# Optimization experiments

Hardware: AMD Instinct MI355X
Metric: run time of the kernel (lower is better)

Reference implementation:

```python
import jax, jax.numpy as jnp
import numpy as np

N_NODES = 50000
N_EDGES = 800000
D = 128
N_LAYERS = 4
NUM_GRAPHS = 128
BN_EPS = 1e-5


def setup_inputs() -> dict:
    key = jax.random.key(0)
    ks = jax.random.split(key, 10)
    x = jax.random.normal(ks[0], (N_NODES, D), dtype=jnp.float32)
    edge_index = jax.random.randint(ks[1], (2, N_EDGES), 0, N_NODES, dtype=jnp.int64)
    batch = jnp.sort(jax.random.randint(ks[2], (N_NODES,), 0, NUM_GRAPHS, dtype=jnp.int64))
    # GINConv MLP params: Linear(D->D), ReLU, Linear(D->D); stacked over layers.
    scale = 1.0 / np.sqrt(D)
    W1 = jax.random.normal(ks[3], (N_LAYERS, D, D), dtype=jnp.float32) * scale
    b1 = jnp.zeros((N_LAYERS, D), dtype=jnp.float32)
    W2 = jax.random.normal(ks[4], (N_LAYERS, D, D), dtype=jnp.float32) * scale
    b2 = jnp.zeros((N_LAYERS, D), dtype=jnp.float32)
    eps = jnp.zeros((N_LAYERS,), dtype=jnp.float32)  # train_eps=True, init 0
    bn_gamma = jnp.ones((N_LAYERS - 1, D), dtype=jnp.float32)
    bn_beta = jnp.zeros((N_LAYERS - 1, D), dtype=jnp.float32)
    return {"x": x, "edge_index": edge_index, "batch": batch,
            "W1": W1, "b1": b1, "W2": W2, "b2": b2, "eps": eps,
            "bn_gamma": bn_gamma, "bn_beta": bn_beta}


def reference(x, edge_index, batch, W1, b1, W2, b2, eps, bn_gamma, bn_beta):
    src, dst = edge_index[0], edge_index[1]
    h = x
    for i in range(N_LAYERS):
        # GINConv: MLP((1+eps)*x_i + sum_{j->i} x_j)
        agg = jax.ops.segment_sum(h[src], dst, num_segments=N_NODES)  # [N, D]
        z = (1.0 + eps[i]) * h + agg
        z = jnp.maximum(z @ W1[i] + b1[i], 0.0) @ W2[i] + b2[i]
        if i < N_LAYERS - 1:
            # BatchNorm1d (training-mode batch statistics) + ReLU
            mu = jnp.mean(z, axis=0)
            var = jnp.var(z, axis=0)
            z = (z - mu) * jax.lax.rsqrt(var + BN_EPS) * bn_gamma[i] + bn_beta[i]
            z = jnp.maximum(z, 0.0)
        h = z
    # global_add_pool
    return jax.ops.segment_sum(h, batch, num_segments=NUM_GRAPHS)  # [G, D]
```

## Files before the change

kernel.cpp:

```cpp
#include <hip/hip_runtime.h>

#define N_NODES 50000
#define N_EDGES 800000
#define D 128
#define NUM_GRAPHS 128

typedef __attribute__((ext_vector_type(8)))  short bfrag8;
typedef __attribute__((ext_vector_type(16))) float f32x16;

__device__ __forceinline__ float4 f4zero() { return make_float4(0.f, 0.f, 0.f, 0.f); }

__device__ __forceinline__ unsigned short f2bf(float f) {
    unsigned u = __float_as_uint(f);
    unsigned r = (u + 0x7fffu + ((u >> 16) & 1u)) >> 16;
    return (unsigned short)r;
}
__device__ __forceinline__ float bf2f(unsigned short b) {
    return __uint_as_float(((unsigned)b) << 16);
}
__device__ __forceinline__ void acc8(float* a, uint4 r) {
    a[0] += __uint_as_float(r.x << 16);
    a[1] += __uint_as_float(r.x & 0xffff0000u);
    a[2] += __uint_as_float(r.y << 16);
    a[3] += __uint_as_float(r.y & 0xffff0000u);
    a[4] += __uint_as_float(r.z << 16);
    a[5] += __uint_as_float(r.z & 0xffff0000u);
    a[6] += __uint_as_float(r.w << 16);
    a[7] += __uint_as_float(r.w & 0xffff0000u);
}

__global__ __launch_bounds__(256) void prep_kernel(
    const float* __restrict__ W1, const float* __restrict__ W2,
    const float* __restrict__ x, short* __restrict__ Wt,
    ushort4* __restrict__ Hb, unsigned* __restrict__ HcDummy,
    int* __restrict__ deg, float* __restrict__ stats,
    float* __restrict__ outZero)
{
    int b = blockIdx.x, t = threadIdx.x;
    if (b < 512) {
        int idx = b * 256 + t;
        int m = idx >> 14, rem = idx & 16383;
        int k = rem >> 7, n = rem & 127;
        const float* W = (m < 4) ? (W1 + (size_t)m * 16384)
                                 : (W2 + (size_t)(m - 4) * 16384);
        Wt[(size_t)m * 16384 + n * 128 + k] = (short)f2bf(W[k * 128 + n]);
    } else if (b < 6762) {
        int i = (b - 512) * 256 + t;
        float4 v = ((const float4*)x)[i];
        Hb[i] = make_ushort4(f2bf(v.x), f2bf(v.y), f2bf(v.z), f2bf(v.w));
    } else if (b < 6958) {
        int i = (b - 6762) * 256 + t;
        if (i < N_NODES) deg[i] = 0;
    } else if (b < 6982) {
        int i = (b - 6958) * 256 + t;
        stats[i] = 0.f;
    } else if (b < 7046) {
        int i = (b - 6982) * 256 + t;
        outZero[i] = 0.f;
    } else {
        if (t < 64)       ((unsigned*)Hb)[(size_t)N_NODES * 64 + t] = 0u;
        else if (t < 128) HcDummy[t - 64] = 0u;
    }
}

__global__ __launch_bounds__(256) void hist_kernel(
    const int* __restrict__ dst, int* __restrict__ deg,
    unsigned short* __restrict__ edge_pos)
{
    int e = blockIdx.x * 256 + threadIdx.x;
    if (e < N_EDGES) edge_pos[e] = (unsigned short)atomicAdd(&deg[dst[e]], 1);
}

__global__ __launch_bounds__(256) void scan_block_kernel(
    const int* __restrict__ deg, int* __restrict__ row_ptr,
    int* __restrict__ blockSum)
{
    __shared__ int wsum[4];
    int t = threadIdx.x, b = blockIdx.x;
    int i = b * 256 + t;
    int v = (i < N_NODES) ? ((deg[i] + 7) & ~7) : 0;
    int lane = t & 63, wid = t >> 6;
    #pragma unroll
    for (int off = 1; off < 64; off <<= 1) {
        int u = __shfl_up(v, off, 64);
        if (lane >= off) v += u;
    }
    if (lane == 63) wsum[wid] = v;
    __syncthreads();
    int add = 0;
    for (int w = 0; w < wid; ++w) add += wsum[w];
    v += add;
    if (i < N_NODES) row_ptr[i + 1] = v;
    if (t == 255) blockSum[b] = v;
}

__global__ __launch_bounds__(256) void scan_fixup_kernel(
    const int* __restrict__ blockSum, int* __restrict__ row_ptr, int nb)
{
    __shared__ int wsum[4];
    __shared__ int sbuf[256];
    int t = threadIdx.x, b = blockIdx.x;
    int v = (t < nb) ? blockSum[t] : 0;
    int lane = t & 63, wid = t >> 6;
    #pragma unroll
    for (int off = 1; off < 64; off <<= 1) {
        int u = __shfl_up(v, off, 64);
        if (lane >= off) v += u;
    }
    if (lane == 63) wsum[wid] = v;
    __syncthreads();
    int add = 0;
    for (int w = 0; w < wid; ++w) add += wsum[w];
    sbuf[t] = v + add;
    __syncthreads();
    if (b == 0 && t == 0) row_ptr[0] = 0;
    if (b > 0) {
        int off = sbuf[b - 1];
        int i = b * 256 + t;
        if (i < N_NODES) row_ptr[i + 1] += off;
    }
}

__global__ __launch_bounds__(256) void fill_kernel(
    const int* __restrict__ src, const int* __restrict__ dst,
    const int* __restrict__ row_ptr, const unsigned short* __restrict__ edge_pos,
    const int* __restrict__ deg, unsigned short* __restrict__ csr_src)
{
    int b = blockIdx.x, t = threadIdx.x;
    if (b < 3125) {
        int e = b * 256 + t;
        if (e < N_EDGES)
            csr_src[row_ptr[dst[e]] + (int)edge_pos[e]] = (unsigned short)src[e];
    } else {
        int n = (b - 3125) * 256 + t;
        if (n < N_NODES) {
            int e0 = row_ptr[n] + deg[n];
            int e1 = row_ptr[n + 1];
            for (int j = e0; j < e1; ++j)
                csr_src[j] = (unsigned short)N_NODES;
        }
    }
}

__global__ __launch_bounds__(256) void bnapply_kernel(
    uint4* __restrict__ H, const float* __restrict__ stats,
    const float* __restrict__ gamma, const float* __restrict__ beta)
{
    __shared__ float sa[128], sb[128];
    int tid = threadIdx.x;
    if (tid < 128) {
        float s = 0.f, q = 0.f;
        #pragma unroll
        for (int k = 0; k < 8; ++k) {
            s += stats[k * 256 + tid];
            q += stats[k * 256 + 128 + tid];
        }
        const float invN = 1.0f / (float)N_NODES;
        float m = s * invN;
        float a = gamma[tid] * rsqrtf(q * invN - m * m + 1e-5f);
        sa[tid] = a;
        sb[tid] = beta[tid] - m * a;
    }
    __syncthreads();
    int id = blockIdx.x * 256 + tid;
    int c0 = (id & 15) * 8;
    uint4 u = H[id];
    float lo, hi;
    lo = fmaxf(sa[c0 + 0] * __uint_as_float(u.x << 16)          + sb[c0 + 0], 0.f);
    hi = fmaxf(sa[c0 + 1] * __uint_as_float(u.x & 0xffff0000u) + sb[c0 + 1], 0.f);
    u.x = (unsigned)f2bf(lo) | ((unsigned)f2bf(hi) << 16);
    lo = fmaxf(sa[c0 + 2] * __uint_as_float(u.y << 16)          + sb[c0 + 2], 0.f);
    hi = fmaxf(sa[c0 + 3] * __uint_as_float(u.y & 0xffff0000u) + sb[c0 + 3], 0.f);
    u.y = (unsigned)f2bf(lo) | ((unsigned)f2bf(hi) << 16);
    lo = fmaxf(sa[c0 + 4] * __uint_as_float(u.z << 16)          + sb[c0 + 4], 0.f);
    hi = fmaxf(sa[c0 + 5] * __uint_as_float(u.z & 0xffff0000u) + sb[c0 + 5], 0.f);
    u.z = (unsigned)f2bf(lo) | ((unsigned)f2bf(hi) << 16);
    lo = fmaxf(sa[c0 + 6] * __uint_as_float(u.w << 16)          + sb[c0 + 6], 0.f);
    hi = fmaxf(sa[c0 + 7] * __uint_as_float(u.w & 0xffff0000u) + sb[c0 + 7], 0.f);
    u.w = (unsigned)f2bf(lo) | ((unsigned)f2bf(hi) << 16);
    H[id] = u;
}

__global__ __launch_bounds__(256, 3) void layer_kernel(
    const ushort* __restrict__ Hin,
    const int* __restrict__ row_ptr,
    const unsigned short* __restrict__ csr,
    const float* __restrict__ epsp,
    const short* __restrict__ Wt1,
    const short* __restrict__ Wt2,
    const float* __restrict__ bias1,
    const float* __restrict__ bias2,
    ushort* __restrict__ Hout,
    float* __restrict__ statsBase,
    const int* __restrict__ batch,
    float* __restrict__ poolOut,
    int M)
{
    __shared__ __align__(16) short Wlds[128 * 128];
    __shared__ __align__(16) short zlds[2][32 * 128];
    __shared__ float ssum[128];
    __shared__ float ssq[128];

    const int tid  = threadIdx.x;
    const int wv   = tid >> 6;
    const int lane = tid & 63;
    const int half = lane >> 5;
    const int ln   = lane & 31;
    const int rg   = wv & 1;
    const int ch   = wv >> 1;
    const int row0 = blockIdx.x * 64 + rg * 32;
    const bool doStats = (statsBase != nullptr);
    if (doStats && tid < 128) { ssum[tid] = 0.f; ssq[tid] = 0.f; }

    short* zw = &zlds[rg][0];

    {
        const uint4* H4 = (const uint4*)Hin;
        const float eps1 = 1.0f + *epsp;
        const int gl = tid & 15;
        #pragma unroll
        for (int it = 0; it < 4; ++it) {
            int r = it * 16 + (tid >> 4);
            int node = blockIdx.x * 64 + r;
            float acc[8] = {0.f, 0.f, 0.f, 0.f, 0.f, 0.f, 0.f, 0.f};
            if (node < M) {
                uint4 hv = H4[(size_t)node * 16 + gl];
                acc[0] = eps1 * __uint_as_float(hv.x << 16);
                acc[1] = eps1 * __uint_as_float(hv.x & 0xffff0000u);
                acc[2] = eps1 * __uint_as_float(hv.y << 16);
                acc[3] = eps1 * __uint_as_float(hv.y & 0xffff0000u);
                acc[4] = eps1 * __uint_as_float(hv.z << 16);
                acc[5] = eps1 * __uint_as_float(hv.z & 0xffff0000u);
                acc[6] = eps1 * __uint_as_float(hv.w << 16);
                acc[7] = eps1 * __uint_as_float(hv.w & 0xffff0000u);
                int beg = row_ptr[node], end = row_ptr[node + 1];
                int base = beg;
                int idx = (int)csr[base + gl];
                while (base < end) {
                    int nb = base + 16;
                    int nidx = 0;
                    if (nb < end) nidx = (int)csr[nb + gl];
                    int cnt = end - base;
                    int s0 = __shfl(idx, 0, 16), s1 = __shfl(idx, 1, 16);
                    int s2 = __shfl(idx, 2, 16), s3 = __shfl(idx, 3, 16);
                    int s4 = __shfl(idx, 4, 16), s5 = __shfl(idx, 5, 16);
                    int s6 = __shfl(idx, 6, 16), s7 = __shfl(idx, 7, 16);
                    uint4 u0 = H4[(size_t)s0 * 16 + gl];
                    uint4 u1 = H4[(size_t)s1 * 16 + gl];
                    uint4 u2 = H4[(size_t)s2 * 16 + gl];
                    uint4 u3 = H4[(size_t)s3 * 16 + gl];
                    uint4 u4 = H4[(size_t)s4 * 16 + gl];
                    uint4 u5 = H4[(size_t)s5 * 16 + gl];
                    uint4 u6 = H4[(size_t)s6 * 16 + gl];
                    uint4 u7 = H4[(size_t)s7 * 16 + gl];
                    if (cnt > 8) {
                        int t0 = __shfl(idx,  8, 16), t1 = __shfl(idx,  9, 16);
                        int t2 = __shfl(idx, 10, 16), t3 = __shfl(idx, 11, 16);
                        int t4 = __shfl(idx, 12, 16), t5 = __shfl(idx, 13, 16);
                        int t6 = __shfl(idx, 14, 16), t7 = __shfl(idx, 15, 16);
                        uint4 w0 = H4[(size_t)t0 * 16 + gl];
                        uint4 w1 = H4[(size_t)t1 * 16 + gl];
                        uint4 w2 = H4[(size_t)t2 * 16 + gl];
                        uint4 w3 = H4[(size_t)t3 * 16 + gl];
                        uint4 w4 = H4[(size_t)t4 * 16 + gl];
                        uint4 w5 = H4[(size_t)t5 * 16 + gl];
                        uint4 w6 = H4[(size_t)t6 * 16 + gl];
                        uint4 w7 = H4[(size_t)t7 * 16 + gl];
                        acc8(acc, u0); acc8(acc, u1); acc8(acc, u2); acc8(acc, u3);
                        acc8(acc, u4); acc8(acc, u5); acc8(acc, u6); acc8(acc, u7);
                        acc8(acc, w0); acc8(acc, w1); acc8(acc, w2); acc8(acc, w3);
                        acc8(acc, w4); acc8(acc, w5); acc8(acc, w6); acc8(acc, w7);
                    } else {
                        acc8(acc, u0); acc8(acc, u1); acc8(acc, u2); acc8(acc, u3);
                        acc8(acc, u4); acc8(acc, u5); acc8(acc, u6); acc8(acc, u7);
                    }
                    idx = nidx; base = nb;
                }
            }
            uint4 o;
            o.x = (unsigned)f2bf(acc[0]) | ((unsigned)f2bf(acc[1]) << 16);
            o.y = (unsigned)f2bf(acc[2]) | ((unsigned)f2bf(acc[3]) << 16);
            o.z = (unsigned)f2bf(acc[4]) | ((unsigned)f2bf(acc[5]) << 16);
            o.w = (unsigned)f2bf(acc[6]) | ((unsigned)f2bf(acc[7]) << 16);
            int rl = r & 31;
            ((uint4*)&zlds[r >> 5][0])[rl * 16 + (gl ^ (rl & 15))] = o;
        }
    }
    __syncthreads();

    bfrag8 af[8];
    #pragma unroll
    for (int kk = 0; kk < 8; ++kk) {
        int c = kk * 2 + half;
        af[kk] = *(const bfrag8*)(zw + ln * 128 + ((c ^ (ln & 15)) << 3));
    }
    {
        const int4* Wg = (const int4*)Wt1;
        int4* Wl = (int4*)Wlds;
        #pragma unroll
        for (int i = 0; i < 8; ++i) {
            int id = i * 256 + tid;
            int n = id >> 4, c = id & 15;
            Wl[n * 16 + (c ^ (n & 15))] = Wg[id];
        }
    }
    __syncthreads();

    {
        f32x16 acc[2];
        #pragma unroll
        for (int ci = 0; ci < 2; ++ci)
            #pragma unroll
            for (int r = 0; r < 16; ++r) acc[ci][r] = 0.f;

        #pragma unroll
        for (int kk = 0; kk < 8; ++kk) {
            #pragma unroll
            for (int ci = 0; ci < 2; ++ci) {
                int n = (ch * 2 + ci) * 32 + ln;
                int c = kk * 2 + half;
                bfrag8 bf = *(const bfrag8*)(Wlds + n * 128 + ((c ^ (n & 15)) << 3));
                acc[ci] = __builtin_amdgcn_mfma_f32_32x32x16_bf16(
                    af[kk], bf, acc[ci], 0, 0, 0);
            }
        }
        #pragma unroll
        for (int ci = 0; ci < 2; ++ci) {
            int col = (ch * 2 + ci) * 32 + ln;
            int cc = col >> 3, co = col & 7;
            float bv = bias1[col];
            #pragma unroll
            for (int r = 0; r < 16; ++r) {
                int rloc = (r & 3) + 8 * (r >> 2) + 4 * half;
                float v = fmaxf(acc[ci][r] + bv, 0.f);
                zw[rloc * 128 + ((cc ^ (rloc & 15)) << 3) + co] = (short)f2bf(v);
            }
        }
    }
    __syncthreads();

    bfrag8 af2[8];
    #pragma unroll
    for (int kk = 0; kk < 8; ++kk) {
        int c = kk * 2 + half;
        af2[kk] = *(const bfrag8*)(zw + ln * 128 + ((c ^ (ln & 15)) << 3));
    }
    {
        const int4* Wg = (const int4*)Wt2;
        int4* Wl = (int4*)Wlds;
        #pragma unroll
        for (int i = 0; i < 8; ++i) {
            int id = i * 256 + tid;
            int n = id >> 4, c = id & 15;
            Wl[n * 16 + (c ^ (n & 15))] = Wg[id];
        }
    }
    __syncthreads();

    {
        f32x16 acc[2];
        #pragma unroll
        for (int ci = 0; ci < 2; ++ci)
            #pragma unroll
            for (int r = 0; r < 16; ++r) acc[ci][r] = 0.f;

        #pragma unroll
        for (int kk = 0; kk < 8; ++kk) {
            #pragma unroll
            for (int ci = 0; ci < 2; ++ci) {
                int n = (ch * 2 + ci) * 32 + ln;
                int c = kk * 2 + half;
                bfrag8 bf = *(const bfrag8*)(Wlds + n * 128 + ((c ^ (n & 15)) << 3));
                acc[ci] = __builtin_amdgcn_mfma_f32_32x32x16_bf16(
                    af2[kk], bf, acc[ci], 0, 0, 0);
            }
        }
        #pragma unroll
        for (int ci = 0; ci < 2; ++ci) {
            int col = (ch * 2 + ci) * 32 + ln;
            int cc = col >> 3, co = col & 7;
            float bv = bias2[col];
            float s = 0.f, sq = 0.f;
            #pragma unroll
            for (int r = 0; r < 16; ++r) {
                int rloc = (r & 3) + 8 * (r >> 2) + 4 * half;
                float v = acc[ci][r] + bv;
                zw[rloc * 128 + ((cc ^ (rloc & 15)) << 3) + co] = (short)f2bf(v);
                if (row0 + rloc < M) { s += v; sq += v * v; }
            }
            if (doStats) {
                s  += __shfl_xor(s, 32);
                sq += __shfl_xor(sq, 32);
                if (half == 0) {
                    atomicAdd(&ssum[col], s);
                    atomicAdd(&ssq[col], sq);
                }
            }
        }
    }
    __syncthreads();

    if (poolOut == nullptr) {
        int4* Ho = (int4*)Hout;
        #pragma unroll
        for (int i = 0; i < 4; ++i) {
            int id = i * 256 + tid;
            int r = id >> 4, c = id & 15;
            int rl = r & 31;
            int grow = blockIdx.x * 64 + r;
            if (grow < M)
                Ho[(size_t)grow * 16 + c] =
                    ((const int4*)&zlds[r >> 5][0])[rl * 16 + (c ^ (rl & 15))];
        }
    } else {
        int c4 = tid & 31;
        int rl8 = tid >> 5;
        int cc = c4 >> 1, co = (c4 & 1) * 4;
        float4 ap = f4zero();
        int gcur = -1;
        for (int i = rl8; i < 64; i += 8) {
            int grow = blockIdx.x * 64 + i;
            if (grow >= M) break;
            int g = batch[grow];
            if (g != gcur) {
                if (gcur >= 0) {
                    float* o = poolOut + gcur * D + c4 * 4;
                    atomicAdd(o + 0, ap.x); atomicAdd(o + 1, ap.y);
                    atomicAdd(o + 2, ap.z); atomicAdd(o + 3, ap.w);
                }
                gcur = g; ap = f4zero();
            }
            const short* zr = &zlds[i >> 5][0];
            int rl = i & 31;
            const ushort4 u = *(const ushort4*)
                ((const ushort*)(zr + rl * 128 + ((cc ^ (rl & 15)) << 3) + co));
            ap.x += bf2f(u.x); ap.y += bf2f(u.y);
            ap.z += bf2f(u.z); ap.w += bf2f(u.w);
        }
        if (gcur >= 0) {
            float* o = poolOut + gcur * D + c4 * 4;
            atomicAdd(o + 0, ap.x); atomicAdd(o + 1, ap.y);
            atomicAdd(o + 2, ap.z); atomicAdd(o + 3, ap.w);
        }
    }
    if (doStats && tid < 128) {
        float* slot = statsBase + (size_t)(blockIdx.x & 7) * 256;
        atomicAdd(&slot[tid],       ssum[tid]);
        atomicAdd(&slot[128 + tid], ssq[tid]);
    }
}

extern "C" void kernel_launch(void* const* d_in, const int* in_sizes, int n_in,
                              void* d_out, int out_size, void* d_ws, size_t ws_size,
                              hipStream_t stream)
{
    const float* x     = (const float*)d_in[0];
    const int*   ei    = (const int*)d_in[1];
    const int*   batch = (const int*)d_in[2];
    const float* W1    = (const float*)d_in[3];
    const float* b1    = (const float*)d_in[4];
    const float* W2    = (const float*)d_in[5];
    const float* b2    = (const float*)d_in[6];
    const float* eps   = (const float*)d_in[7];
    const float* gamma = (const float*)d_in[8];
    const float* beta  = (const float*)d_in[9];
    float* out = (float*)d_out;

    unsigned short* Hb  = (unsigned short*)d_ws;
    unsigned short* Hc  = Hb + (size_t)(N_NODES + 1) * D;
    float* stats    = (float*)(Hc + (size_t)(N_NODES + 1) * D);
    int*   deg      = (int*)(stats + 3 * 2048);
    int*   row_ptr  = deg + N_NODES;
    int*   blockSum = row_ptr + N_NODES + 1;
    unsigned short* edge_pos = (unsigned short*)(blockSum + 256);
    unsigned short* csr_src  = edge_pos + N_EDGES;
    short* Wt       = (short*)(csr_src + N_EDGES + 7 * N_NODES + 16);

    const int* src = ei;
    const int* dst = ei + N_EDGES;

    const int edgeBlocks = (N_EDGES + 255) / 256;
    const int scanBlocks = (N_NODES + 255) / 256;
    const int bnBlocks   = (N_NODES * 16) / 256;
    const int gemmBlocks = (N_NODES + 63) / 64;

    prep_kernel<<<7047, 256, 0, stream>>>(W1, W2, x, Wt, (ushort4*)Hb,
                                          (unsigned*)(Hc + (size_t)N_NODES * D),
                                          deg, stats, out);
    hist_kernel<<<edgeBlocks, 256, 0, stream>>>(dst, deg, edge_pos);
    scan_block_kernel<<<scanBlocks, 256, 0, stream>>>(deg, row_ptr, blockSum);
    scan_fixup_kernel<<<scanBlocks, 256, 0, stream>>>(blockSum, row_ptr, scanBlocks);
    fill_kernel<<<edgeBlocks + scanBlocks, 256, 0, stream>>>(
        src, dst, row_ptr, edge_pos, deg, csr_src);

    unsigned short* Hin  = Hb;
    unsigned short* HoutB = Hc;
    for (int layer = 0; layer < 4; ++layer) {
        const bool bn = (layer < 3);
        if (layer > 0) {
            bnapply_kernel<<<bnBlocks, 256, 0, stream>>>(
                (uint4*)Hin, stats + (size_t)(layer - 1) * 2048,
                gamma + (size_t)(layer - 1) * D, beta + (size_t)(layer - 1) * D);
        }
        layer_kernel<<<gemmBlocks, 256, 0, stream>>>(
            Hin, row_ptr, csr_src, eps + layer,
            Wt + (size_t)layer * 16384, Wt + (size_t)(4 + layer) * 16384,
            b1 + (size_t)layer * D, b2 + (size_t)layer * D, HoutB,
            bn ? stats + (size_t)layer * 2048 : nullptr,
            bn ? nullptr : batch,
            bn ? nullptr : out, N_NODES);
        unsigned short* tmp = Hin; Hin = HoutB; HoutB = tmp;
    }
}
```

Baseline: 342.7 us.

## Read MLP weights directly from global memory instead of staging in LDS

Removes the 32KB shared-memory weight buffer and the cooperative copies of W1 and W2 into it. Each lane now loads its B-fragments straight from global memory, relying on L1/L2 caching of the small weight matrices. The launch-bounds occupancy hint is raised from 3 to 6 blocks, since LDS use per block drops sharply. This trades LDS staging and a barrier's worth of copy work for more global or cache loads per MFMA, and for higher register pressure under the tighter occupancy target.

```diff
diff --git a/kernel.cpp b/kernel.cpp
--- a/kernel.cpp
+++ b/kernel.cpp
@@ -181,7 +181,7 @@
     H[id] = u;
 }
 
-__global__ __launch_bounds__(256, 3) void layer_kernel(
+__global__ __launch_bounds__(256, 6) void layer_kernel(
     const ushort* __restrict__ Hin,
     const int* __restrict__ row_ptr,
     const unsigned short* __restrict__ csr,
@@ -196,7 +196,6 @@
     float* __restrict__ poolOut,
     int M)
 {
-    __shared__ __align__(16) short Wlds[128 * 128];
     __shared__ __align__(16) short zlds[2][32 * 128];
     __shared__ float ssum[128];
     __shared__ float ssq[128];
@@ -294,16 +293,6 @@
         int c = kk * 2 + half;
         af[kk] = *(const bfrag8*)(zw + ln * 128 + ((c ^ (ln & 15)) << 3));
     }
-    {
-        const int4* Wg = (const int4*)Wt1;
-        int4* Wl = (int4*)Wlds;
-        #pragma unroll
-        for (int i = 0; i < 8; ++i) {
-            int id = i * 256 + tid;
-            int n = id >> 4, c = id & 15;
-            Wl[n * 16 + (c ^ (n & 15))] = Wg[id];
-        }
-    }
     __syncthreads();
 
     {
@@ -313,13 +302,12 @@
             #pragma unroll
             for (int r = 0; r < 16; ++r) acc[ci][r] = 0.f;
 
+        const short* Wb = Wt1 + (size_t)(ch * 64 + ln) * 128 + half * 8;
         #pragma unroll
         for (int kk = 0; kk < 8; ++kk) {
             #pragma unroll
             for (int ci = 0; ci < 2; ++ci) {
-                int n = (ch * 2 + ci) * 32 + ln;
-                int c = kk * 2 + half;
-                bfrag8 bf = *(const bfrag8*)(Wlds + n * 128 + ((c ^ (n & 15)) << 3));
+                bfrag8 bf = *(const bfrag8*)(Wb + ci * 32 * 128 + kk * 16);
                 acc[ci] = __builtin_amdgcn_mfma_f32_32x32x16_bf16(
                     af[kk], bf, acc[ci], 0, 0, 0);
             }
@@ -345,16 +333,6 @@
         int c = kk * 2 + half;
         af2[kk] = *(const bfrag8*)(zw + ln * 128 + ((c ^ (ln & 15)) << 3));
     }
-    {
-        const int4* Wg = (const int4*)Wt2;
-        int4* Wl = (int4*)Wlds;
-        #pragma unroll
-        for (int i = 0; i < 8; ++i) {
-            int id = i * 256 + tid;
-            int n = id >> 4, c = id & 15;
-            Wl[n * 16 + (c ^ (n & 15))] = Wg[id];
-        }
-    }
     __syncthreads();
 
     {
@@ -364,13 +342,12 @@
             #pragma unroll
             for (int r = 0; r < 16; ++r) acc[ci][r] = 0.f;
 
+        const short* Wb = Wt2 + (size_t)(ch * 64 + ln) * 128 + half * 8;
         #pragma unroll
         for (int kk = 0; kk < 8; ++kk) {
             #pragma unroll
             for (int ci = 0; ci < 2; ++ci) {
-                int n = (ch * 2 + ci) * 32 + ln;
-                int c = kk * 2 + half;
-                bfrag8 bf = *(const bfrag8*)(Wlds + n * 128 + ((c ^ (n & 15)) << 3));
+                bfrag8 bf = *(const bfrag8*)(Wb + ci * 32 * 128 + kk * 16);
                 acc[ci] = __builtin_amdgcn_mfma_f32_32x32x16_bf16(
                     af2[kk], bf, acc[ci], 0, 0, 0);
             }
```

Measured after the change: 464.8 us. +35.6%, slower.
